# Optimization experiments

Hardware: AMD Instinct MI355X
Metric: run time of the kernel (lower is better)

Reference implementation:

```python
import jax, jax.numpy as jnp
import numpy as np

N_NODES = 50000
N_EDGES = 800000  # includes N_NODES self-loops so every node has in-degree >= 1
D_IN = 64
D_OUT = 64


def setup_inputs() -> dict:
    key = jax.random.key(0)
    k_feat, k_src, k_dst, k_wt, k_wp = jax.random.split(key, 5)
    feat = jax.random.normal(k_feat, (N_NODES, D_IN), dtype=jnp.float32)
    n_rand = N_EDGES - N_NODES
    loops = jnp.arange(N_NODES, dtype=jnp.int64)
    src = jnp.concatenate([loops, jax.random.randint(k_src, (n_rand,), 0, N_NODES, dtype=jnp.int64)])
    dst = jnp.concatenate([loops, jax.random.randint(k_dst, (n_rand,), 0, N_NODES, dtype=jnp.int64)])
    scale = 1.0 / np.sqrt(D_IN)
    W_theta = jax.random.normal(k_wt, (D_IN, D_OUT), dtype=jnp.float32) * scale
    b_theta = jnp.zeros((D_OUT,), dtype=jnp.float32)
    W_phi = jax.random.normal(k_wp, (D_IN, D_OUT), dtype=jnp.float32) * scale
    b_phi = jnp.zeros((D_OUT,), dtype=jnp.float32)
    return {"feat": feat, "src": src, "dst": dst,
            "W_theta": W_theta, "b_theta": b_theta,
            "W_phi": W_phi, "b_phi": b_phi}


def reference(feat, src, dst, W_theta, b_theta, W_phi, b_phi):
    # Per-edge message: theta(x_dst - x_src)  [fn.v_sub_u then Dense theta]
    diff = feat[dst] - feat[src]                       # [E, D_in]
    theta_e = diff @ W_theta + b_theta                 # [E, D_out]
    # Per-destination-node term: phi(x_dst)  [Dense phi]
    phi = feat @ W_phi + b_phi                         # [N, D_out]
    e = theta_e + phi[dst]                             # [E, D_out]  (fn.e_add_v)
    # Scatter-max aggregation by destination node (fn.max)
    out = jax.ops.segment_max(e, dst, num_segments=feat.shape[0])  # [N, D_out]
    return out
```

## Files before the change

### kernel.cpp

```cpp
#include <hip/hip_runtime.h>
#include <hip/hip_bf16.h>

#define N_NODES 50000
#define N_EDGES 800000
#define D 64
#define NB 1563
#define BCAP 1024
#define CHUNK_E 2048
#define NSC 391
#define NSTRIP 3125
#define GEMM_BLKS 196
#define NWAVES 784
#define SPW 4
#define MSTR 65

typedef __attribute__((ext_vector_type(8))) short short8v;
typedef __attribute__((ext_vector_type(4))) float float4v;

__device__ __forceinline__ float b2f(unsigned short h) {
    return __uint_as_float(((unsigned)h) << 16);
}
__device__ __forceinline__ unsigned short f2b(float f) {
    __hip_bfloat16 t = __float2bfloat16(f);
    return *reinterpret_cast<unsigned short*>(&t);
}
__device__ __forceinline__ short f2bs(float f) { return (short)f2b(f); }
__device__ __forceinline__ unsigned f2ord(float f) {
    unsigned u = __float_as_uint(f);
    return (u & 0x80000000u) ? ~u : (u | 0x80000000u);
}
__device__ __forceinline__ float ord2f(unsigned o) {
    return __uint_as_float((o & 0x80000000u) ? (o ^ 0x80000000u) : ~o);
}

__global__ __launch_bounds__(256)
void setup(const void* __restrict__ featv, const void* __restrict__ srcv,
           const void* __restrict__ Wtv, const void* __restrict__ btv,
           const void* __restrict__ Wpv, const void* __restrict__ bpv,
           unsigned* __restrict__ flags, unsigned* __restrict__ c_cur,
           unsigned short* __restrict__ WTfrag, unsigned short* __restrict__ WPfrag,
           float* __restrict__ bias_sum) {
    __shared__ unsigned sf[2];
    const int t = threadIdx.x;
    if (t < 64) {
        const unsigned short* p = (const unsigned short*)featv;
        float x = b2f(p[2 * t]);
        float a = fabsf(x);
        bool insane = !(a <= 64.f) || (x != 0.f && a < 9.3132e-10f);
        unsigned long long m = __ballot(insane);
        if (t == 0) sf[0] = (__popcll(m) >= 8) ? 1u : 0u;
    } else if (t < 128) {
        const int* s32 = (const int*)srcv;
        int v = s32[2 * (t - 64) + 1];
        unsigned long long m = __ballot(v == 0);
        if (t == 64) sf[1] = (__popcll(m) >= 32) ? 1u : 0u;
    }
    __syncthreads();
    const unsigned fp32mode = sf[0];
    if (t < 2) flags[t] = sf[t];
    for (int i = t; i < NB; i += 256) c_cur[i] = 0;
#pragma unroll
    for (int i = 0; i < 16; ++i) {
        int e = i * 256 + t;
        int k = e >> 6, n = e & 63;
        float vt, vp;
        if (fp32mode) {
            vt = ((const float*)Wtv)[e];
            vp = ((const float*)Wpv)[e];
        } else {
            vt = b2f(((const unsigned short*)Wtv)[e]);
            vp = b2f(((const unsigned short*)Wpv)[e]);
        }
        WTfrag[n * 64 + k] = f2b(vt);
        WPfrag[n * 64 + k] = f2b(vp);
    }
    if (t < 64) {
        if (fp32mode)
            bias_sum[t] = ((const float*)btv)[t] + ((const float*)bpv)[t];
        else
            bias_sum[t] = b2f(((const unsigned short*)btv)[t])
                        + b2f(((const unsigned short*)bpv)[t]);
    }
}

__device__ __forceinline__ void loadA_bf16(const short* F, int w, int m, int q,
                                           short8v& A0, short8v& A1) {
    const short* fr = F + (w * 16 + m) * D + q * 8;
    A0 = *(const short8v*)fr;
    A1 = *(const short8v*)(fr + 32);
}
__device__ __forceinline__ void loadA_raw(const float* F, int w, int m, int q,
                                          float4 r[8]) {
    const float* fr = F + (w * 16 + m) * D + q * 8;
    r[0] = *(const float4*)(fr);      r[1] = *(const float4*)(fr + 4);
    r[2] = *(const float4*)(fr + 32); r[3] = *(const float4*)(fr + 36);
}
__device__ __forceinline__ void cvtA(const float4 r[8], short8v& A0, short8v& A1) {
    A0 = (short8v){f2bs(r[0].x), f2bs(r[0].y), f2bs(r[0].z), f2bs(r[0].w),
                   f2bs(r[1].x), f2bs(r[1].y), f2bs(r[1].z), f2bs(r[1].w)};
    A1 = (short8v){f2bs(r[2].x), f2bs(r[2].y), f2bs(r[2].z), f2bs(r[2].w),
                   f2bs(r[3].x), f2bs(r[3].y), f2bs(r[3].z), f2bs(r[3].w)};
}

__global__ __launch_bounds__(256)
void gemm_scatter(const void* __restrict__ featv,
                  const unsigned short* __restrict__ WTfrag,
                  const unsigned short* __restrict__ WPfrag,
                  const float* __restrict__ bias_sum,
                  const void* __restrict__ srcv, const void* __restrict__ dstv,
                  const unsigned* __restrict__ flags,
                  unsigned* __restrict__ c_cur, unsigned* __restrict__ packed,
                  unsigned short* __restrict__ T16, void* __restrict__ outv) {
    const unsigned fp32mode = flags[0];
    if (blockIdx.x < GEMM_BLKS) {
        const int lane = threadIdx.x & 63;
        const int wid  = threadIdx.x >> 6;
        const int wave = blockIdx.x * 4 + wid;
        const int m = lane & 15, q = lane >> 4;

        const short8v* BT = (const short8v*)WTfrag;
        const short8v* BP = (const short8v*)WPfrag;
        short8v Wt0[4], Wt1[4], Wp0[4], Wp1[4];
        float4 bs4[4];
#pragma unroll
        for (int c = 0; c < 4; ++c) {
            const int col = 16 * c + m;
            Wt0[c] = BT[col * 8 + q];
            Wt1[c] = BT[col * 8 + 4 + q];
            Wp0[c] = BP[col * 8 + q];
            Wp1[c] = BP[col * 8 + 4 + q];
            bs4[c] = *(const float4*)(bias_sum + 16 * c + 4 * q);
        }

        float* Cf  = (float*)outv;
        unsigned short* Ch = (unsigned short*)outv;
        const float* Ff = (const float*)featv;
        const short* Fh = (const short*)featv;

        short8v A0, A1;
        float4 raw[8];
        int w = wave;
        if (fp32mode) { loadA_raw(Ff, min(w, NSTRIP - 1), m, q, raw); cvtA(raw, A0, A1); }
        else          loadA_bf16(Fh, min(w, NSTRIP - 1), m, q, A0, A1);

#pragma unroll
        for (int s = 0; s < SPW; ++s) {
            const int wn = wave + (s + 1) * NWAVES;
            if (s + 1 < SPW) {
                if (fp32mode) loadA_raw(Ff, min(wn, NSTRIP - 1), m, q, raw);
                else          loadA_bf16(Fh, min(wn, NSTRIP - 1), m, q, A0, A1);
            }
            if (w < NSTRIP) {
                short8v Acur0, Acur1;
                if (s + 1 < SPW && !fp32mode) {
                    loadA_bf16(Fh, w, m, q, Acur0, Acur1);
                } else {
                    Acur0 = A0; Acur1 = A1;
                }
                const int node = w * 16 + m;
                unsigned short* Trow = T16 + node * D;
#pragma unroll
                for (int c = 0; c < 4; ++c) {
                    float4v accT = (float4v){0.f, 0.f, 0.f, 0.f};
                    float4v accP = (float4v){bs4[c].x, bs4[c].y, bs4[c].z, bs4[c].w};
                    accT = __builtin_amdgcn_mfma_f32_16x16x32_bf16(Wt0[c], Acur0, accT, 0, 0, 0);
                    accT = __builtin_amdgcn_mfma_f32_16x16x32_bf16(Wt1[c], Acur1, accT, 0, 0, 0);
                    accP = __builtin_amdgcn_mfma_f32_16x16x32_bf16(Wp0[c], Acur0, accP, 0, 0, 0);
                    accP = __builtin_amdgcn_mfma_f32_16x16x32_bf16(Wp1[c], Acur1, accP, 0, 0, 0);
                    const int foff = 16 * c + 4 * q;
                    unsigned t0 = (unsigned)f2b(accT[0]) | ((unsigned)f2b(accT[1]) << 16);
                    unsigned t1 = (unsigned)f2b(accT[2]) | ((unsigned)f2b(accT[3]) << 16);
                    *(uint2*)(Trow + foff) = make_uint2(t0, t1);
                    if (fp32mode) {
                        *(float4*)(Cf + node * D + foff) =
                            make_float4(accT[0] + accP[0], accT[1] + accP[1],
                                        accT[2] + accP[2], accT[3] + accP[3]);
                    } else {
                        unsigned c0 = (unsigned)f2b(accT[0] + accP[0])
                                    | ((unsigned)f2b(accT[1] + accP[1]) << 16);
                        unsigned c1 = (unsigned)f2b(accT[2] + accP[2])
                                    | ((unsigned)f2b(accT[3] + accP[3]) << 16);
                        *(uint2*)(Ch + node * D + foff) = make_uint2(c0, c1);
                    }
                }
            }
            w = wn;
            if (fp32mode && s + 1 < SPW) cvtA(raw, A0, A1);
        }
    } else {
        __shared__ unsigned h[NB];
        const int t = threadIdx.x;
        for (int i = t; i < NB; i += 256) h[i] = 0;
        __syncthreads();
        const unsigned idx64 = flags[1];
        const int base = (blockIdx.x - GEMM_BLKS) * CHUNK_E;
        unsigned pk[CHUNK_E / 256];
#pragma unroll
        for (int j = 0; j < CHUNK_E / 256; ++j) {
            int e = base + j * 256 + t;
            unsigned p = 0xFFFFFFFFu;
            if (e < N_EDGES) {
                int s, d;
                if (idx64) {
                    s = (int)((const long long*)srcv)[e];
                    d = (int)((const long long*)dstv)[e];
                } else {
                    s = ((const int*)srcv)[e];
                    d = ((const int*)dstv)[e];
                }
                s = min(max(s, 0), N_NODES - 1);
                d = min(max(d, 0), N_NODES - 1);
                if (s != d) {
                    p = ((unsigned)d << 16) | (unsigned)s;
                    atomicAdd(&h[d >> 5], 1u);
                }
            }
            pk[j] = p;
        }
        __syncthreads();
        for (int i = t; i < NB; i += 256) {
            unsigned c = h[i];
            h[i] = c ? atomicAdd(&c_cur[i], c) : 0u;
        }
        __syncthreads();
#pragma unroll
        for (int j = 0; j < CHUNK_E / 256; ++j) {
            unsigned p = pk[j];
            if (p != 0xFFFFFFFFu) {
                unsigned bkt = p >> 21;
                unsigned pos = atomicAdd(&h[bkt], 1u);
                if (pos < BCAP)
                    packed[bkt * BCAP + pos] = p;
            }
        }
    }
}

__global__ __launch_bounds__(256, 8)
void bucket_min(const unsigned* __restrict__ c_cur, const unsigned* __restrict__ packed,
                const unsigned short* __restrict__ T16, const unsigned* __restrict__ flags,
                void* __restrict__ outv) {
    __shared__ unsigned mn[32 * MSTR];
    const unsigned fp32mode = flags[0];
    const int t = threadIdx.x;
    const int b = blockIdx.x;
    const int node0 = b << 5;
    for (int sl = t; sl < 32 * 16; sl += 256) {
        const int row = sl >> 4;
        const int f4 = (sl & 15) << 2;
        unsigned* mp = &mn[row * MSTR + f4];
        if (node0 + row < N_NODES) {
            uint2 v = *(const uint2*)(T16 + (node0 + row) * D + f4);
            mp[0] = f2ord(b2f((unsigned short)v.x));
            mp[1] = f2ord(b2f((unsigned short)(v.x >> 16)));
            mp[2] = f2ord(b2f((unsigned short)v.y));
            mp[3] = f2ord(b2f((unsigned short)(v.y >> 16)));
        } else {
            mp[0] = mp[1] = mp[2] = mp[3] = 0xFFFFFFFFu;
        }
    }
    __syncthreads();
    const int cnt = min((int)c_cur[b], BCAP);
    const unsigned* pb = packed + b * BCAP;
    const int lane = t & 63, wv = t >> 6;
    const int g = lane >> 3;
    const int fh = (lane & 7) << 3;
    const int fu = (lane & 7) << 3;
    int i = wv * 8 + g;
    for (; i + 32 < cnt; i += 64) {
        unsigned p0 = pb[i], p1 = pb[i + 32];
        uint4 v0 = *(const uint4*)(T16 + (int)(p0 & 0xFFFFu) * D + fh);
        uint4 v1 = *(const uint4*)(T16 + (int)(p1 & 0xFFFFu) * D + fh);
        unsigned* m0p = &mn[(int)((p0 >> 16) & 31u) * MSTR + fu];
        unsigned* m1p = &mn[(int)((p1 >> 16) & 31u) * MSTR + fu];
        atomicMin(m0p + 0, f2ord(b2f((unsigned short)v0.x)));
        atomicMin(m0p + 1, f2ord(b2f((unsigned short)(v0.x >> 16))));
        atomicMin(m0p + 2, f2ord(b2f((unsigned short)v0.y)));
        atomicMin(m0p + 3, f2ord(b2f((unsigned short)(v0.y >> 16))));
        atomicMin(m0p + 4, f2ord(b2f((unsigned short)v0.z)));
        atomicMin(m0p + 5, f2ord(b2f((unsigned short)(v0.z >> 16))));
        atomicMin(m0p + 6, f2ord(b2f((unsigned short)v0.w)));
        atomicMin(m0p + 7, f2ord(b2f((unsigned short)(v0.w >> 16))));
        atomicMin(m1p + 0, f2ord(b2f((unsigned short)v1.x)));
        atomicMin(m1p + 1, f2ord(b2f((unsigned short)(v1.x >> 16))));
        atomicMin(m1p + 2, f2ord(b2f((unsigned short)v1.y)));
        atomicMin(m1p + 3, f2ord(b2f((unsigned short)(v1.y >> 16))));
        atomicMin(m1p + 4, f2ord(b2f((unsigned short)v1.z)));
        atomicMin(m1p + 5, f2ord(b2f((unsigned short)(v1.z >> 16))));
        atomicMin(m1p + 6, f2ord(b2f((unsigned short)v1.w)));
        atomicMin(m1p + 7, f2ord(b2f((unsigned short)(v1.w >> 16))));
    }
    for (; i < cnt; i += 32) {
        unsigned p0 = pb[i];
        uint4 v0 = *(const uint4*)(T16 + (int)(p0 & 0xFFFFu) * D + fh);
        unsigned* m0p = &mn[(int)((p0 >> 16) & 31u) * MSTR + fu];
        atomicMin(m0p + 0, f2ord(b2f((unsigned short)v0.x)));
        atomicMin(m0p + 1, f2ord(b2f((unsigned short)(v0.x >> 16))));
        atomicMin(m0p + 2, f2ord(b2f((unsigned short)v0.y)));
        atomicMin(m0p + 3, f2ord(b2f((unsigned short)(v0.y >> 16))));
        atomicMin(m0p + 4, f2ord(b2f((unsigned short)v0.z)));
        atomicMin(m0p + 5, f2ord(b2f((unsigned short)(v0.z >> 16))));
        atomicMin(m0p + 6, f2ord(b2f((unsigned short)v0.w)));
        atomicMin(m0p + 7, f2ord(b2f((unsigned short)(v0.w >> 16))));
    }
    __syncthreads();
    for (int sl = t; sl < 32 * 16; sl += 256) {
        const int row = sl >> 4;
        const int node = node0 + row;
        if (node >= N_NODES) continue;
        const int f4 = (sl & 15) << 2;
        const unsigned* mp = &mn[row * MSTR + f4];
        float m0 = ord2f(mp[0]), m1 = ord2f(mp[1]);
        float m2 = ord2f(mp[2]), m3 = ord2f(mp[3]);
        if (fp32mode) {
            float4* C = (float4*)((float*)outv + node * D + f4);
            float4 c = *C;
            *C = make_float4(c.x - m0, c.y - m1, c.z - m2, c.w - m3);
        } else {
            unsigned short* C = (unsigned short*)outv + node * D + f4;
            uint2 c = *(uint2*)C;
            unsigned lo = (unsigned)f2b(b2f((unsigned short)c.x) - m0)
                        | ((unsigned)f2b(b2f((unsigned short)(c.x >> 16)) - m1) << 16);
            unsigned hi = (unsigned)f2b(b2f((unsigned short)c.y) - m2)
                        | ((unsigned)f2b(b2f((unsigned short)(c.y >> 16)) - m3) << 16);
            *(uint2*)C = make_uint2(lo, hi);
        }
    }
}

extern "C" void kernel_launch(void* const* d_in, const int* in_sizes, int n_in,
                              void* d_out, int out_size, void* d_ws, size_t ws_size,
                              hipStream_t stream) {
    char* p = (char*)d_ws;
    unsigned*       flags    = (unsigned*)p;
    unsigned*       c_cur    = (unsigned*)(p + 256);
    unsigned*       packed   = (unsigned*)(p + 8448);
    unsigned short* T16      = (unsigned short*)(p + 8448 + 6402048);
    unsigned short* WTfrag   = (unsigned short*)(p + 8448 + 6402048 + 6400000);
    unsigned short* WPfrag   = (unsigned short*)(p + 8448 + 6402048 + 6400000 + 8192);
    float*          bias_sum = (float*)(p + 8448 + 6402048 + 6400000 + 16384);

    setup<<<1, 256, 0, stream>>>(d_in[0], d_in[1], d_in[3], d_in[4], d_in[5], d_in[6],
                                 flags, c_cur, WTfrag, WPfrag, bias_sum);
    gemm_scatter<<<GEMM_BLKS + NSC, 256, 0, stream>>>(d_in[0], WTfrag, WPfrag, bias_sum,
                                                      d_in[1], d_in[2], flags,
                                                      c_cur, packed, T16, d_out);
    bucket_min<<<NB, 256, 0, stream>>>(c_cur, packed, T16, flags, d_out);
}
```

Baseline: 124.2 us.

## Fuse setup, GEMM/scatter and bucket-min into one cooperative persistent kernel

Replaces the three-kernel sequence with a single cooperative kernel using grid.sync between phases: setup of weight fragments and counters, then GEMM plus edge bucketing, then a dynamic work-queue loop over destination buckets computing the max via LDS atomics. The aim is to remove two kernel launch boundaries and the tail effects between them, and to balance the bucket phase with an atomic cursor. It adds grid-wide barrier cost, limits occupancy to a fixed grid of 1024 blocks, and falls back to the old path if the cooperative launch fails.

```diff
diff --git a/kernel.cpp b/kernel.cpp
--- a/kernel.cpp
+++ b/kernel.cpp
@@ -1,18 +1,25 @@
 #include <hip/hip_runtime.h>
 #include <hip/hip_bf16.h>
+#include <hip/hip_cooperative_groups.h>
+
+namespace cg = cooperative_groups;
 
 #define N_NODES 50000
 #define N_EDGES 800000
 #define D 64
 #define NB 1563
 #define BCAP 1024
+#define NSTRIP 3125
+#define MSTR 65
+#define GRID_B 1024
+#define GEMM_B 391
+#define SCAT_B 633
+#define EPB 1264
 #define CHUNK_E 2048
 #define NSC 391
-#define NSTRIP 3125
 #define GEMM_BLKS 196
 #define NWAVES 784
 #define SPW 4
-#define MSTR 65
 
 typedef __attribute__((ext_vector_type(8))) short short8v;
 typedef __attribute__((ext_vector_type(4))) float float4v;
@@ -31,6 +38,284 @@
 }
 __device__ __forceinline__ float ord2f(unsigned o) {
     return __uint_as_float((o & 0x80000000u) ? (o ^ 0x80000000u) : ~o);
+}
+
+__device__ __forceinline__ void loadA_bf16(const short* F, int w, int m, int q,
+                                           short8v& A0, short8v& A1) {
+    const short* fr = F + (w * 16 + m) * D + q * 8;
+    A0 = *(const short8v*)fr;
+    A1 = *(const short8v*)(fr + 32);
+}
+__device__ __forceinline__ void loadA_raw(const float* F, int w, int m, int q,
+                                          float4 r[8]) {
+    const float* fr = F + (w * 16 + m) * D + q * 8;
+    r[0] = *(const float4*)(fr);      r[1] = *(const float4*)(fr + 4);
+    r[2] = *(const float4*)(fr + 32); r[3] = *(const float4*)(fr + 36);
+}
+__device__ __forceinline__ void cvtA(const float4 r[8], short8v& A0, short8v& A1) {
+    A0 = (short8v){f2bs(r[0].x), f2bs(r[0].y), f2bs(r[0].z), f2bs(r[0].w),
+                   f2bs(r[1].x), f2bs(r[1].y), f2bs(r[1].z), f2bs(r[1].w)};
+    A1 = (short8v){f2bs(r[2].x), f2bs(r[2].y), f2bs(r[2].z), f2bs(r[2].w),
+                   f2bs(r[3].x), f2bs(r[3].y), f2bs(r[3].z), f2bs(r[3].w)};
+}
+
+__global__ __launch_bounds__(256, 4)
+void fused(const void* __restrict__ featv, const void* __restrict__ srcv,
+           const void* __restrict__ dstv, const void* __restrict__ Wtv,
+           const void* __restrict__ btv, const void* __restrict__ Wpv,
+           const void* __restrict__ bpv,
+           unsigned* __restrict__ c_cur, unsigned* __restrict__ packed,
+           unsigned short* __restrict__ T16,
+           unsigned short* __restrict__ WTfrag, unsigned short* __restrict__ WPfrag,
+           float* __restrict__ bias_sum, unsigned* __restrict__ cursor,
+           void* __restrict__ outv) {
+    __shared__ unsigned sh[32 * MSTR];
+    __shared__ unsigned sf[4];
+    cg::grid_group grid = cg::this_grid();
+    const int t = threadIdx.x;
+    const int b = blockIdx.x;
+
+    if (t < 64) {
+        const unsigned short* p = (const unsigned short*)featv;
+        float x = b2f(p[2 * t]);
+        float a = fabsf(x);
+        bool insane = !(a <= 64.f) || (x != 0.f && a < 9.3132e-10f);
+        unsigned long long m = __ballot(insane);
+        if (t == 0) sf[0] = (__popcll(m) >= 8) ? 1u : 0u;
+    } else if (t < 128) {
+        const int* s32 = (const int*)srcv;
+        int v = s32[2 * (t - 64) + 1];
+        unsigned long long m = __ballot(v == 0);
+        if (t == 64) sf[1] = (__popcll(m) >= 32) ? 1u : 0u;
+    }
+    __syncthreads();
+    const unsigned fp32mode = sf[0];
+    const unsigned idx64 = sf[1];
+
+    if (b == 0) {
+#pragma unroll
+        for (int i = 0; i < 16; ++i) {
+            int e = i * 256 + t;
+            int k = e >> 6, n = e & 63;
+            float vt, vp;
+            if (fp32mode) {
+                vt = ((const float*)Wtv)[e];
+                vp = ((const float*)Wpv)[e];
+            } else {
+                vt = b2f(((const unsigned short*)Wtv)[e]);
+                vp = b2f(((const unsigned short*)Wpv)[e]);
+            }
+            WTfrag[n * 64 + k] = f2b(vt);
+            WPfrag[n * 64 + k] = f2b(vp);
+        }
+        if (t < 64) {
+            if (fp32mode)
+                bias_sum[t] = ((const float*)btv)[t] + ((const float*)bpv)[t];
+            else
+                bias_sum[t] = b2f(((const unsigned short*)btv)[t])
+                            + b2f(((const unsigned short*)bpv)[t]);
+        }
+    } else if (b <= 7) {
+        int i = (b - 1) * 256 + t;
+        if (i < NB) c_cur[i] = 0;
+    } else if (b == 8 && t == 0) {
+        *cursor = 0;
+    }
+    grid.sync();
+
+    if (b < GEMM_B) {
+        const int lane = t & 63, wid = t >> 6;
+        const int m = lane & 15, q = lane >> 4;
+        const short8v* BT = (const short8v*)WTfrag;
+        const short8v* BP = (const short8v*)WPfrag;
+        short8v Wt0[4], Wt1[4], Wp0[4], Wp1[4];
+        float4 bs4[4];
+#pragma unroll
+        for (int c = 0; c < 4; ++c) {
+            const int col = 16 * c + m;
+            Wt0[c] = BT[col * 8 + q];
+            Wt1[c] = BT[col * 8 + 4 + q];
+            Wp0[c] = BP[col * 8 + q];
+            Wp1[c] = BP[col * 8 + 4 + q];
+            bs4[c] = *(const float4*)(bias_sum + 16 * c + 4 * q);
+        }
+        float* Cf  = (float*)outv;
+        unsigned short* Ch = (unsigned short*)outv;
+#pragma unroll
+        for (int si = 0; si < 2; ++si) {
+            const int w = b * 8 + wid * 2 + si;
+            if (w < NSTRIP) {
+                short8v A0, A1;
+                if (fp32mode) {
+                    float4 raw[8];
+                    loadA_raw((const float*)featv, w, m, q, raw);
+                    cvtA(raw, A0, A1);
+                } else {
+                    loadA_bf16((const short*)featv, w, m, q, A0, A1);
+                }
+                const int node = w * 16 + m;
+                unsigned short* Trow = T16 + node * D;
+#pragma unroll
+                for (int c = 0; c < 4; ++c) {
+                    float4v accT = (float4v){0.f, 0.f, 0.f, 0.f};
+                    float4v accP = (float4v){bs4[c].x, bs4[c].y, bs4[c].z, bs4[c].w};
+                    accT = __builtin_amdgcn_mfma_f32_16x16x32_bf16(Wt0[c], A0, accT, 0, 0, 0);
+                    accT = __builtin_amdgcn_mfma_f32_16x16x32_bf16(Wt1[c], A1, accT, 0, 0, 0);
+                    accP = __builtin_amdgcn_mfma_f32_16x16x32_bf16(Wp0[c], A0, accP, 0, 0, 0);
+                    accP = __builtin_amdgcn_mfma_f32_16x16x32_bf16(Wp1[c], A1, accP, 0, 0, 0);
+                    const int foff = 16 * c + 4 * q;
+                    unsigned t0 = (unsigned)f2b(accT[0]) | ((unsigned)f2b(accT[1]) << 16);
+                    unsigned t1 = (unsigned)f2b(accT[2]) | ((unsigned)f2b(accT[3]) << 16);
+                    *(uint2*)(Trow + foff) = make_uint2(t0, t1);
+                    if (fp32mode) {
+                        *(float4*)(Cf + node * D + foff) =
+                            make_float4(accT[0] + accP[0], accT[1] + accP[1],
+                                        accT[2] + accP[2], accT[3] + accP[3]);
+                    } else {
+                        unsigned c0 = (unsigned)f2b(accT[0] + accP[0])
+                                    | ((unsigned)f2b(accT[1] + accP[1]) << 16);
+                        unsigned c1 = (unsigned)f2b(accT[2] + accP[2])
+                                    | ((unsigned)f2b(accT[3] + accP[3]) << 16);
+                        *(uint2*)(Ch + node * D + foff) = make_uint2(c0, c1);
+                    }
+                }
+            }
+        }
+    } else {
+        const int base = (b - GEMM_B) * EPB;
+        const int eend = min(base + EPB, N_EDGES);
+        for (int i = t; i < NB; i += 256) sh[i] = 0;
+        __syncthreads();
+        unsigned pk[5];
+#pragma unroll
+        for (int j = 0; j < 5; ++j) {
+            int e = base + j * 256 + t;
+            unsigned p = 0xFFFFFFFFu;
+            if (e < eend) {
+                int s, d;
+                if (idx64) {
+                    s = (int)((const long long*)srcv)[e];
+                    d = (int)((const long long*)dstv)[e];
+                } else {
+                    s = ((const int*)srcv)[e];
+                    d = ((const int*)dstv)[e];
+                }
+                s = min(max(s, 0), N_NODES - 1);
+                d = min(max(d, 0), N_NODES - 1);
+                if (s != d) {
+                    p = ((unsigned)d << 16) | (unsigned)s;
+                    atomicAdd(&sh[d >> 5], 1u);
+                }
+            }
+            pk[j] = p;
+        }
+        __syncthreads();
+        for (int i = t; i < NB; i += 256) {
+            unsigned c = sh[i];
+            sh[i] = c ? atomicAdd(&c_cur[i], c) : 0u;
+        }
+        __syncthreads();
+#pragma unroll
+        for (int j = 0; j < 5; ++j) {
+            unsigned p = pk[j];
+            if (p != 0xFFFFFFFFu) {
+                unsigned bkt = p >> 21;
+                unsigned pos = atomicAdd(&sh[bkt], 1u);
+                if (pos < BCAP)
+                    packed[bkt * BCAP + pos] = p;
+            }
+        }
+    }
+    grid.sync();
+
+    const int lane = t & 63, wv = t >> 6;
+    const int g = lane >> 3;
+    const int fh = (lane & 7) << 3;
+    for (;;) {
+        if (t == 0) sf[2] = atomicAdd(cursor, 1u);
+        __syncthreads();
+        const unsigned bb = sf[2];
+        if (bb >= NB) break;
+        const int node0 = (int)bb << 5;
+        for (int sl = t; sl < 32 * 16; sl += 256) {
+            const int row = sl >> 4;
+            const int f4 = (sl & 15) << 2;
+            unsigned* mp = &sh[row * MSTR + f4];
+            if (node0 + row < N_NODES) {
+                uint2 v = *(const uint2*)(T16 + (node0 + row) * D + f4);
+                mp[0] = f2ord(b2f((unsigned short)v.x));
+                mp[1] = f2ord(b2f((unsigned short)(v.x >> 16)));
+                mp[2] = f2ord(b2f((unsigned short)v.y));
+                mp[3] = f2ord(b2f((unsigned short)(v.y >> 16)));
+            } else {
+                mp[0] = mp[1] = mp[2] = mp[3] = 0xFFFFFFFFu;
+            }
+        }
+        __syncthreads();
+        const int cnt = min((int)c_cur[bb], BCAP);
+        const unsigned* pb = packed + bb * BCAP;
+        int i = wv * 8 + g;
+        for (; i + 32 < cnt; i += 64) {
+            unsigned p0 = pb[i], p1 = pb[i + 32];
+            uint4 v0 = *(const uint4*)(T16 + (int)(p0 & 0xFFFFu) * D + fh);
+            uint4 v1 = *(const uint4*)(T16 + (int)(p1 & 0xFFFFu) * D + fh);
+            unsigned* m0p = &sh[(int)((p0 >> 16) & 31u) * MSTR + fh];
+            unsigned* m1p = &sh[(int)((p1 >> 16) & 31u) * MSTR + fh];
+            atomicMin(m0p + 0, f2ord(b2f((unsigned short)v0.x)));
+            atomicMin(m0p + 1, f2ord(b2f((unsigned short)(v0.x >> 16))));
+            atomicMin(m0p + 2, f2ord(b2f((unsigned short)v0.y)));
+            atomicMin(m0p + 3, f2ord(b2f((unsigned short)(v0.y >> 16))));
+            atomicMin(m0p + 4, f2ord(b2f((unsigned short)v0.z)));
+            atomicMin(m0p + 5, f2ord(b2f((unsigned short)(v0.z >> 16))));
+            atomicMin(m0p + 6, f2ord(b2f((unsigned short)v0.w)));
+            atomicMin(m0p + 7, f2ord(b2f((unsigned short)(v0.w >> 16))));
+            atomicMin(m1p + 0, f2ord(b2f((unsigned short)v1.x)));
+            atomicMin(m1p + 1, f2ord(b2f((unsigned short)(v1.x >> 16))));
+            atomicMin(m1p + 2, f2ord(b2f((unsigned short)v1.y)));
+            atomicMin(m1p + 3, f2ord(b2f((unsigned short)(v1.y >> 16))));
+            atomicMin(m1p + 4, f2ord(b2f((unsigned short)v1.z)));
+            atomicMin(m1p + 5, f2ord(b2f((unsigned short)(v1.z >> 16))));
+            atomicMin(m1p + 6, f2ord(b2f((unsigned short)v1.w)));
+            atomicMin(m1p + 7, f2ord(b2f((unsigned short)(v1.w >> 16))));
+        }
+        for (; i < cnt; i += 32) {
+            unsigned p0 = pb[i];
+            uint4 v0 = *(const uint4*)(T16 + (int)(p0 & 0xFFFFu) * D + fh);
+            unsigned* m0p = &sh[(int)((p0 >> 16) & 31u) * MSTR + fh];
+            atomicMin(m0p + 0, f2ord(b2f((unsigned short)v0.x)));
+            atomicMin(m0p + 1, f2ord(b2f((unsigned short)(v0.x >> 16))));
+            atomicMin(m0p + 2, f2ord(b2f((unsigned short)v0.y)));
+            atomicMin(m0p + 3, f2ord(b2f((unsigned short)(v0.y >> 16))));
+            atomicMin(m0p + 4, f2ord(b2f((unsigned short)v0.z)));
+            atomicMin(m0p + 5, f2ord(b2f((unsigned short)(v0.z >> 16))));
+            atomicMin(m0p + 6, f2ord(b2f((unsigned short)v0.w)));
+            atomicMin(m0p + 7, f2ord(b2f((unsigned short)(v0.w >> 16))));
+        }
+        __syncthreads();
+        for (int sl = t; sl < 32 * 16; sl += 256) {
+            const int row = sl >> 4;
+            const int node = node0 + row;
+            if (node >= N_NODES) continue;
+            const int f4 = (sl & 15) << 2;
+            const unsigned* mp = &sh[row * MSTR + f4];
+            float m0 = ord2f(mp[0]), m1 = ord2f(mp[1]);
+            float m2 = ord2f(mp[2]), m3 = ord2f(mp[3]);
+            if (fp32mode) {
+                float4* C = (float4*)((float*)outv + node * D + f4);
+                float4 c = *C;
+                *C = make_float4(c.x - m0, c.y - m1, c.z - m2, c.w - m3);
+            } else {
+                unsigned short* C = (unsigned short*)outv + node * D + f4;
+                uint2 c = *(uint2*)C;
+                unsigned lo = (unsigned)f2b(b2f((unsigned short)c.x) - m0)
+                            | ((unsigned)f2b(b2f((unsigned short)(c.x >> 16)) - m1) << 16);
+                unsigned hi = (unsigned)f2b(b2f((unsigned short)c.y) - m2)
+                            | ((unsigned)f2b(b2f((unsigned short)(c.y >> 16)) - m3) << 16);
+                *(uint2*)C = make_uint2(lo, hi);
+            }
+        }
+        __syncthreads();
+    }
 }
 
 __global__ __launch_bounds__(256)
@@ -83,25 +368,6 @@
     }
 }
 
-__device__ __forceinline__ void loadA_bf16(const short* F, int w, int m, int q,
-                                           short8v& A0, short8v& A1) {
-    const short* fr = F + (w * 16 + m) * D + q * 8;
-    A0 = *(const short8v*)fr;
-    A1 = *(const short8v*)(fr + 32);
-}
-__device__ __forceinline__ void loadA_raw(const float* F, int w, int m, int q,
-                                          float4 r[8]) {
-    const float* fr = F + (w * 16 + m) * D + q * 8;
-    r[0] = *(const float4*)(fr);      r[1] = *(const float4*)(fr + 4);
-    r[2] = *(const float4*)(fr + 32); r[3] = *(const float4*)(fr + 36);
-}
-__device__ __forceinline__ void cvtA(const float4 r[8], short8v& A0, short8v& A1) {
-    A0 = (short8v){f2bs(r[0].x), f2bs(r[0].y), f2bs(r[0].z), f2bs(r[0].w),
-                   f2bs(r[1].x), f2bs(r[1].y), f2bs(r[1].z), f2bs(r[1].w)};
-    A1 = (short8v){f2bs(r[2].x), f2bs(r[2].y), f2bs(r[2].z), f2bs(r[2].w),
-                   f2bs(r[3].x), f2bs(r[3].y), f2bs(r[3].z), f2bs(r[3].w)};
-}
-
 __global__ __launch_bounds__(256)
 void gemm_scatter(const void* __restrict__ featv,
                   const unsigned short* __restrict__ WTfrag,
@@ -117,7 +383,6 @@
         const int wid  = threadIdx.x >> 6;
         const int wave = blockIdx.x * 4 + wid;
         const int m = lane & 15, q = lane >> 4;
-
         const short8v* BT = (const short8v*)WTfrag;
         const short8v* BP = (const short8v*)WPfrag;
         short8v Wt0[4], Wt1[4], Wp0[4], Wp1[4];
@@ -131,18 +396,15 @@
             Wp1[c] = BP[col * 8 + 4 + q];
             bs4[c] = *(const float4*)(bias_sum + 16 * c + 4 * q);
         }
-
         float* Cf  = (float*)outv;
         unsigned short* Ch = (unsigned short*)outv;
         const float* Ff = (const float*)featv;
         const short* Fh = (const short*)featv;
-
         short8v A0, A1;
         float4 raw[8];
         int w = wave;
         if (fp32mode) { loadA_raw(Ff, min(w, NSTRIP - 1), m, q, raw); cvtA(raw, A0, A1); }
         else          loadA_bf16(Fh, min(w, NSTRIP - 1), m, q, A0, A1);
-
 #pragma unroll
         for (int s = 0; s < SPW; ++s) {
             const int wn = wave + (s + 1) * NWAVES;
@@ -265,14 +527,13 @@
     const int lane = t & 63, wv = t >> 6;
     const int g = lane >> 3;
     const int fh = (lane & 7) << 3;
-    const int fu = (lane & 7) << 3;
     int i = wv * 8 + g;
     for (; i + 32 < cnt; i += 64) {
         unsigned p0 = pb[i], p1 = pb[i + 32];
         uint4 v0 = *(const uint4*)(T16 + (int)(p0 & 0xFFFFu) * D + fh);
         uint4 v1 = *(const uint4*)(T16 + (int)(p1 & 0xFFFFu) * D + fh);
-        unsigned* m0p = &mn[(int)((p0 >> 16) & 31u) * MSTR + fu];
-        unsigned* m1p = &mn[(int)((p1 >> 16) & 31u) * MSTR + fu];
+        unsigned* m0p = &mn[(int)((p0 >> 16) & 31u) * MSTR + fh];
+        unsigned* m1p = &mn[(int)((p1 >> 16) & 31u) * MSTR + fh];
         atomicMin(m0p + 0, f2ord(b2f((unsigned short)v0.x)));
         atomicMin(m0p + 1, f2ord(b2f((unsigned short)(v0.x >> 16))));
         atomicMin(m0p + 2, f2ord(b2f((unsigned short)v0.y)));
@@ -293,7 +554,7 @@
     for (; i < cnt; i += 32) {
         unsigned p0 = pb[i];
         uint4 v0 = *(const uint4*)(T16 + (int)(p0 & 0xFFFFu) * D + fh);
-        unsigned* m0p = &mn[(int)((p0 >> 16) & 31u) * MSTR + fu];
+        unsigned* m0p = &mn[(int)((p0 >> 16) & 31u) * MSTR + fh];
         atomicMin(m0p + 0, f2ord(b2f((unsigned short)v0.x)));
         atomicMin(m0p + 1, f2ord(b2f((unsigned short)(v0.x >> 16))));
         atomicMin(m0p + 2, f2ord(b2f((unsigned short)v0.y)));
@@ -339,11 +600,30 @@
     unsigned short* WTfrag   = (unsigned short*)(p + 8448 + 6402048 + 6400000);
     unsigned short* WPfrag   = (unsigned short*)(p + 8448 + 6402048 + 6400000 + 8192);
     float*          bias_sum = (float*)(p + 8448 + 6402048 + 6400000 + 16384);
-
-    setup<<<1, 256, 0, stream>>>(d_in[0], d_in[1], d_in[3], d_in[4], d_in[5], d_in[6],
-                                 flags, c_cur, WTfrag, WPfrag, bias_sum);
-    gemm_scatter<<<GEMM_BLKS + NSC, 256, 0, stream>>>(d_in[0], WTfrag, WPfrag, bias_sum,
-                                                      d_in[1], d_in[2], flags,
-                                                      c_cur, packed, T16, d_out);
-    bucket_min<<<NB, 256, 0, stream>>>(c_cur, packed, T16, flags, d_out);
-}
+    unsigned*       cursor   = (unsigned*)(p + 8448 + 6402048 + 6400000 + 16640);
+
+    const void* featv = d_in[0];
+    const void* srcv  = d_in[1];
+    const void* dstv  = d_in[2];
+    const void* Wtv   = d_in[3];
+    const void* btv   = d_in[4];
+    const void* Wpv   = d_in[5];
+    const void* bpv   = d_in[6];
+    void* outv = d_out;
+
+    void* kargs[] = { (void*)&featv, (void*)&srcv, (void*)&dstv, (void*)&Wtv,
+                      (void*)&btv, (void*)&Wpv, (void*)&bpv,
+                      (void*)&c_cur, (void*)&packed, (void*)&T16,
+                      (void*)&WTfrag, (void*)&WPfrag, (void*)&bias_sum,
+                      (void*)&cursor, (void*)&outv };
+    hipError_t err = hipLaunchCooperativeKernel((const void*)fused, dim3(GRID_B),
+                                                dim3(256), kargs, 0, stream);
+    if (err != hipSuccess) {
+        setup<<<1, 256, 0, stream>>>(featv, srcv, Wtv, btv, Wpv, bpv,
+                                     flags, c_cur, WTfrag, WPfrag, bias_sum);
+        gemm_scatter<<<GEMM_BLKS + NSC, 256, 0, stream>>>(featv, WTfrag, WPfrag, bias_sum,
+                                                          srcv, dstv, flags,
+                                                          c_cur, packed, T16, outv);
+        bucket_min<<<NB, 256, 0, stream>>>(c_cur, packed, T16, flags, outv);
+    }
+}
```

Result: slower. 340.6 us (+174.2%).

## Fold setup kernel into gemm_scatter and halve scatter block count

Applied to the files above, without the earlier changes.

Removes the single-block setup kernel. Each GEMM block now stages the weights and bias into LDS itself, every block recomputes the dtype/index-width flags locally, and c_cur is zeroed with a memset. This cuts one serialized launch and the global round trip through the weight-fragment buffers. It also doubles the edges per scatter block (half as many blocks) and batches the per-bucket atomicAdd reservations into registers. In exchange, every block repeats the flag detection and weight staging, and with fewer scatter blocks each block does longer serial work.

```diff
diff --git a/kernel.cpp b/kernel.cpp
--- a/kernel.cpp
+++ b/kernel.cpp
@@ -6,13 +6,15 @@
 #define D 64
 #define NB 1563
 #define BCAP 1024
-#define CHUNK_E 2048
-#define NSC 391
+#define CHUNK_E 4096
+#define NSC 196
 #define NSTRIP 3125
 #define GEMM_BLKS 196
 #define NWAVES 784
 #define SPW 4
 #define MSTR 65
+#define WLSTR 72
+#define NRES 7
 
 typedef __attribute__((ext_vector_type(8))) short short8v;
 typedef __attribute__((ext_vector_type(4))) float float4v;
@@ -24,7 +26,6 @@
     __hip_bfloat16 t = __float2bfloat16(f);
     return *reinterpret_cast<unsigned short*>(&t);
 }
-__device__ __forceinline__ short f2bs(float f) { return (short)f2b(f); }
 __device__ __forceinline__ unsigned f2ord(float f) {
     unsigned u = __float_as_uint(f);
     return (u & 0x80000000u) ? ~u : (u | 0x80000000u);
@@ -34,102 +35,80 @@
 }
 
 __global__ __launch_bounds__(256)
-void setup(const void* __restrict__ featv, const void* __restrict__ srcv,
-           const void* __restrict__ Wtv, const void* __restrict__ btv,
-           const void* __restrict__ Wpv, const void* __restrict__ bpv,
-           unsigned* __restrict__ flags, unsigned* __restrict__ c_cur,
-           unsigned short* __restrict__ WTfrag, unsigned short* __restrict__ WPfrag,
-           float* __restrict__ bias_sum) {
+void gemm_scatter(const void* __restrict__ featv,
+                  const void* __restrict__ srcv, const void* __restrict__ dstv,
+                  const void* __restrict__ Wtv, const void* __restrict__ btv,
+                  const void* __restrict__ Wpv, const void* __restrict__ bpv,
+                  unsigned* __restrict__ c_cur, unsigned* __restrict__ packed,
+                  unsigned short* __restrict__ T16, void* __restrict__ outv) {
+    __shared__ __align__(16) unsigned short wt_l[64 * WLSTR];
+    __shared__ __align__(16) unsigned short wp_l[64 * WLSTR];
+    __shared__ __align__(16) float bias_l[64];
+    __shared__ unsigned h[NB];
     __shared__ unsigned sf[2];
     const int t = threadIdx.x;
+
     if (t < 64) {
         const unsigned short* p = (const unsigned short*)featv;
         float x = b2f(p[2 * t]);
         float a = fabsf(x);
         bool insane = !(a <= 64.f) || (x != 0.f && a < 9.3132e-10f);
-        unsigned long long m = __ballot(insane);
-        if (t == 0) sf[0] = (__popcll(m) >= 8) ? 1u : 0u;
+        unsigned long long mm = __ballot(insane);
+        if (t == 0) sf[0] = (__popcll(mm) >= 8) ? 1u : 0u;
     } else if (t < 128) {
         const int* s32 = (const int*)srcv;
         int v = s32[2 * (t - 64) + 1];
-        unsigned long long m = __ballot(v == 0);
-        if (t == 64) sf[1] = (__popcll(m) >= 32) ? 1u : 0u;
+        unsigned long long mm = __ballot(v == 0);
+        if (t == 64) sf[1] = (__popcll(mm) >= 32) ? 1u : 0u;
     }
     __syncthreads();
     const unsigned fp32mode = sf[0];
-    if (t < 2) flags[t] = sf[t];
-    for (int i = t; i < NB; i += 256) c_cur[i] = 0;
-#pragma unroll
-    for (int i = 0; i < 16; ++i) {
-        int e = i * 256 + t;
-        int k = e >> 6, n = e & 63;
-        float vt, vp;
+    const unsigned idx64 = sf[1];
+
+    if (blockIdx.x < GEMM_BLKS) {
         if (fp32mode) {
-            vt = ((const float*)Wtv)[e];
-            vp = ((const float*)Wpv)[e];
+#pragma unroll
+            for (int i = 0; i < 16; ++i) {
+                int e = i * 256 + t;
+                int k = e >> 6, n = e & 63;
+                wt_l[n * WLSTR + k] = f2b(((const float*)Wtv)[e]);
+                wp_l[n * WLSTR + k] = f2b(((const float*)Wpv)[e]);
+            }
         } else {
-            vt = b2f(((const unsigned short*)Wtv)[e]);
-            vp = b2f(((const unsigned short*)Wpv)[e]);
-        }
-        WTfrag[n * 64 + k] = f2b(vt);
-        WPfrag[n * 64 + k] = f2b(vp);
-    }
-    if (t < 64) {
-        if (fp32mode)
-            bias_sum[t] = ((const float*)btv)[t] + ((const float*)bpv)[t];
-        else
-            bias_sum[t] = b2f(((const unsigned short*)btv)[t])
-                        + b2f(((const unsigned short*)bpv)[t]);
-    }
-}
-
-__device__ __forceinline__ void loadA_bf16(const short* F, int w, int m, int q,
-                                           short8v& A0, short8v& A1) {
-    const short* fr = F + (w * 16 + m) * D + q * 8;
-    A0 = *(const short8v*)fr;
-    A1 = *(const short8v*)(fr + 32);
-}
-__device__ __forceinline__ void loadA_raw(const float* F, int w, int m, int q,
-                                          float4 r[8]) {
-    const float* fr = F + (w * 16 + m) * D + q * 8;
-    r[0] = *(const float4*)(fr);      r[1] = *(const float4*)(fr + 4);
-    r[2] = *(const float4*)(fr + 32); r[3] = *(const float4*)(fr + 36);
-}
-__device__ __forceinline__ void cvtA(const float4 r[8], short8v& A0, short8v& A1) {
-    A0 = (short8v){f2bs(r[0].x), f2bs(r[0].y), f2bs(r[0].z), f2bs(r[0].w),
-                   f2bs(r[1].x), f2bs(r[1].y), f2bs(r[1].z), f2bs(r[1].w)};
-    A1 = (short8v){f2bs(r[2].x), f2bs(r[2].y), f2bs(r[2].z), f2bs(r[2].w),
-                   f2bs(r[3].x), f2bs(r[3].y), f2bs(r[3].z), f2bs(r[3].w)};
-}
-
-__global__ __launch_bounds__(256)
-void gemm_scatter(const void* __restrict__ featv,
-                  const unsigned short* __restrict__ WTfrag,
-                  const unsigned short* __restrict__ WPfrag,
-                  const float* __restrict__ bias_sum,
-                  const void* __restrict__ srcv, const void* __restrict__ dstv,
-                  const unsigned* __restrict__ flags,
-                  unsigned* __restrict__ c_cur, unsigned* __restrict__ packed,
-                  unsigned short* __restrict__ T16, void* __restrict__ outv) {
-    const unsigned fp32mode = flags[0];
-    if (blockIdx.x < GEMM_BLKS) {
-        const int lane = threadIdx.x & 63;
-        const int wid  = threadIdx.x >> 6;
+#pragma unroll
+            for (int i = 0; i < 16; ++i) {
+                int e = i * 256 + t;
+                int k = e >> 6, n = e & 63;
+                wt_l[n * WLSTR + k] = ((const unsigned short*)Wtv)[e];
+                wp_l[n * WLSTR + k] = ((const unsigned short*)Wpv)[e];
+            }
+        }
+        if (t < 64) {
+            float bt_, bp_;
+            if (fp32mode) {
+                bt_ = ((const float*)btv)[t];
+                bp_ = ((const float*)bpv)[t];
+            } else {
+                bt_ = b2f(((const unsigned short*)btv)[t]);
+                bp_ = b2f(((const unsigned short*)bpv)[t]);
+            }
+            bias_l[t] = bt_ + bp_;
+        }
+        __syncthreads();
+
+        const int lane = t & 63, wid = t >> 6;
         const int wave = blockIdx.x * 4 + wid;
         const int m = lane & 15, q = lane >> 4;
-
-        const short8v* BT = (const short8v*)WTfrag;
-        const short8v* BP = (const short8v*)WPfrag;
         short8v Wt0[4], Wt1[4], Wp0[4], Wp1[4];
         float4 bs4[4];
 #pragma unroll
         for (int c = 0; c < 4; ++c) {
             const int col = 16 * c + m;
-            Wt0[c] = BT[col * 8 + q];
-            Wt1[c] = BT[col * 8 + 4 + q];
-            Wp0[c] = BP[col * 8 + q];
-            Wp1[c] = BP[col * 8 + 4 + q];
-            bs4[c] = *(const float4*)(bias_sum + 16 * c + 4 * q);
+            Wt0[c] = *(const short8v*)&wt_l[col * WLSTR + q * 8];
+            Wt1[c] = *(const short8v*)&wt_l[col * WLSTR + 32 + q * 8];
+            Wp0[c] = *(const short8v*)&wp_l[col * WLSTR + q * 8];
+            Wp1[c] = *(const short8v*)&wp_l[col * WLSTR + 32 + q * 8];
+            bs4[c] = *(const float4*)&bias_l[16 * c + 4 * q];
         }
 
         float* Cf  = (float*)outv;
@@ -140,20 +119,44 @@
         short8v A0, A1;
         float4 raw[8];
         int w = wave;
-        if (fp32mode) { loadA_raw(Ff, min(w, NSTRIP - 1), m, q, raw); cvtA(raw, A0, A1); }
-        else          loadA_bf16(Fh, min(w, NSTRIP - 1), m, q, A0, A1);
+        {
+            int wc = min(w, NSTRIP - 1);
+            const short* fr = Fh + (wc * 16 + m) * D + q * 8;
+            const float* frf = Ff + (wc * 16 + m) * D + q * 8;
+            if (fp32mode) {
+                raw[0] = *(const float4*)(frf);      raw[1] = *(const float4*)(frf + 4);
+                raw[2] = *(const float4*)(frf + 32); raw[3] = *(const float4*)(frf + 36);
+                A0 = (short8v){(short)f2b(raw[0].x), (short)f2b(raw[0].y), (short)f2b(raw[0].z), (short)f2b(raw[0].w),
+                               (short)f2b(raw[1].x), (short)f2b(raw[1].y), (short)f2b(raw[1].z), (short)f2b(raw[1].w)};
+                A1 = (short8v){(short)f2b(raw[2].x), (short)f2b(raw[2].y), (short)f2b(raw[2].z), (short)f2b(raw[2].w),
+                               (short)f2b(raw[3].x), (short)f2b(raw[3].y), (short)f2b(raw[3].z), (short)f2b(raw[3].w)};
+            } else {
+                A0 = *(const short8v*)fr;
+                A1 = *(const short8v*)(fr + 32);
+            }
+        }
 
 #pragma unroll
         for (int s = 0; s < SPW; ++s) {
             const int wn = wave + (s + 1) * NWAVES;
             if (s + 1 < SPW) {
-                if (fp32mode) loadA_raw(Ff, min(wn, NSTRIP - 1), m, q, raw);
-                else          loadA_bf16(Fh, min(wn, NSTRIP - 1), m, q, A0, A1);
+                int wc = min(wn, NSTRIP - 1);
+                if (fp32mode) {
+                    const float* frf = Ff + (wc * 16 + m) * D + q * 8;
+                    raw[0] = *(const float4*)(frf);      raw[1] = *(const float4*)(frf + 4);
+                    raw[2] = *(const float4*)(frf + 32); raw[3] = *(const float4*)(frf + 36);
+                } else {
+                    const short* fr = Fh + (wc * 16 + m) * D + q * 8;
+                    A0 = *(const short8v*)fr;
+                    A1 = *(const short8v*)(fr + 32);
+                }
             }
             if (w < NSTRIP) {
                 short8v Acur0, Acur1;
                 if (s + 1 < SPW && !fp32mode) {
-                    loadA_bf16(Fh, w, m, q, Acur0, Acur1);
+                    const short* fr = Fh + (w * 16 + m) * D + q * 8;
+                    Acur0 = *(const short8v*)fr;
+                    Acur1 = *(const short8v*)(fr + 32);
                 } else {
                     Acur0 = A0; Acur1 = A1;
                 }
@@ -185,14 +188,16 @@
                 }
             }
             w = wn;
-            if (fp32mode && s + 1 < SPW) cvtA(raw, A0, A1);
+            if (fp32mode && s + 1 < SPW) {
+                A0 = (short8v){(short)f2b(raw[0].x), (short)f2b(raw[0].y), (short)f2b(raw[0].z), (short)f2b(raw[0].w),
+                               (short)f2b(raw[1].x), (short)f2b(raw[1].y), (short)f2b(raw[1].z), (short)f2b(raw[1].w)};
+                A1 = (short8v){(short)f2b(raw[2].x), (short)f2b(raw[2].y), (short)f2b(raw[2].z), (short)f2b(raw[2].w),
+                               (short)f2b(raw[3].x), (short)f2b(raw[3].y), (short)f2b(raw[3].z), (short)f2b(raw[3].w)};
+            }
         }
     } else {
-        __shared__ unsigned h[NB];
-        const int t = threadIdx.x;
         for (int i = t; i < NB; i += 256) h[i] = 0;
         __syncthreads();
-        const unsigned idx64 = flags[1];
         const int base = (blockIdx.x - GEMM_BLKS) * CHUNK_E;
         unsigned pk[CHUNK_E / 256];
 #pragma unroll
@@ -218,9 +223,24 @@
             pk[j] = p;
         }
         __syncthreads();
-        for (int i = t; i < NB; i += 256) {
-            unsigned c = h[i];
-            h[i] = c ? atomicAdd(&c_cur[i], c) : 0u;
+        {
+            unsigned cc[NRES], off[NRES];
+#pragma unroll
+            for (int r = 0; r < NRES; ++r) {
+                int i = r * 256 + t;
+                cc[r] = (i < NB) ? h[i] : 0u;
+            }
+#pragma unroll
+            for (int r = 0; r < NRES; ++r) {
+                int i = r * 256 + t;
+                off[r] = (i < NB && cc[r]) ? atomicAdd(&c_cur[i], cc[r]) : 0u;
+            }
+            __syncthreads();
+#pragma unroll
+            for (int r = 0; r < NRES; ++r) {
+                int i = r * 256 + t;
+                if (i < NB) h[i] = off[r];
+            }
         }
         __syncthreads();
 #pragma unroll
@@ -238,13 +258,21 @@
 
 __global__ __launch_bounds__(256, 8)
 void bucket_min(const unsigned* __restrict__ c_cur, const unsigned* __restrict__ packed,
-                const unsigned short* __restrict__ T16, const unsigned* __restrict__ flags,
+                const unsigned short* __restrict__ T16, const void* __restrict__ featv,
                 void* __restrict__ outv) {
     __shared__ unsigned mn[32 * MSTR];
-    const unsigned fp32mode = flags[0];
+    __shared__ unsigned sf0;
     const int t = threadIdx.x;
     const int b = blockIdx.x;
     const int node0 = b << 5;
+    if (t < 64) {
+        const unsigned short* p = (const unsigned short*)featv;
+        float x = b2f(p[2 * t]);
+        float a = fabsf(x);
+        bool insane = !(a <= 64.f) || (x != 0.f && a < 9.3132e-10f);
+        unsigned long long mm = __ballot(insane);
+        if (t == 0) sf0 = (__popcll(mm) >= 8) ? 1u : 0u;
+    }
     for (int sl = t; sl < 32 * 16; sl += 256) {
         const int row = sl >> 4;
         const int f4 = (sl & 15) << 2;
@@ -260,19 +288,19 @@
         }
     }
     __syncthreads();
+    const unsigned fp32mode = sf0;
     const int cnt = min((int)c_cur[b], BCAP);
     const unsigned* pb = packed + b * BCAP;
     const int lane = t & 63, wv = t >> 6;
     const int g = lane >> 3;
     const int fh = (lane & 7) << 3;
-    const int fu = (lane & 7) << 3;
     int i = wv * 8 + g;
     for (; i + 32 < cnt; i += 64) {
         unsigned p0 = pb[i], p1 = pb[i + 32];
         uint4 v0 = *(const uint4*)(T16 + (int)(p0 & 0xFFFFu) * D + fh);
         uint4 v1 = *(const uint4*)(T16 + (int)(p1 & 0xFFFFu) * D + fh);
-        unsigned* m0p = &mn[(int)((p0 >> 16) & 31u) * MSTR + fu];
-        unsigned* m1p = &mn[(int)((p1 >> 16) & 31u) * MSTR + fu];
+        unsigned* m0p = &mn[(int)((p0 >> 16) & 31u) * MSTR + fh];
+        unsigned* m1p = &mn[(int)((p1 >> 16) & 31u) * MSTR + fh];
         atomicMin(m0p + 0, f2ord(b2f((unsigned short)v0.x)));
         atomicMin(m0p + 1, f2ord(b2f((unsigned short)(v0.x >> 16))));
         atomicMin(m0p + 2, f2ord(b2f((unsigned short)v0.y)));
@@ -293,7 +321,7 @@
     for (; i < cnt; i += 32) {
         unsigned p0 = pb[i];
         uint4 v0 = *(const uint4*)(T16 + (int)(p0 & 0xFFFFu) * D + fh);
-        unsigned* m0p = &mn[(int)((p0 >> 16) & 31u) * MSTR + fu];
+        unsigned* m0p = &mn[(int)((p0 >> 16) & 31u) * MSTR + fh];
         atomicMin(m0p + 0, f2ord(b2f((unsigned short)v0.x)));
         atomicMin(m0p + 1, f2ord(b2f((unsigned short)(v0.x >> 16))));
         atomicMin(m0p + 2, f2ord(b2f((unsigned short)v0.y)));
@@ -328,22 +356,26 @@
     }
 }
 
+__global__ __launch_bounds__(256)
+void zero_ccur(unsigned* __restrict__ c_cur) {
+    int i = blockIdx.x * 256 + threadIdx.x;
+    if (i < NB) c_cur[i] = 0;
+}
+
 extern "C" void kernel_launch(void* const* d_in, const int* in_sizes, int n_in,
                               void* d_out, int out_size, void* d_ws, size_t ws_size,
                               hipStream_t stream) {
     char* p = (char*)d_ws;
-    unsigned*       flags    = (unsigned*)p;
-    unsigned*       c_cur    = (unsigned*)(p + 256);
-    unsigned*       packed   = (unsigned*)(p + 8448);
-    unsigned short* T16      = (unsigned short*)(p + 8448 + 6402048);
-    unsigned short* WTfrag   = (unsigned short*)(p + 8448 + 6402048 + 6400000);
-    unsigned short* WPfrag   = (unsigned short*)(p + 8448 + 6402048 + 6400000 + 8192);
-    float*          bias_sum = (float*)(p + 8448 + 6402048 + 6400000 + 16384);
-
-    setup<<<1, 256, 0, stream>>>(d_in[0], d_in[1], d_in[3], d_in[4], d_in[5], d_in[6],
-                                 flags, c_cur, WTfrag, WPfrag, bias_sum);
-    gemm_scatter<<<GEMM_BLKS + NSC, 256, 0, stream>>>(d_in[0], WTfrag, WPfrag, bias_sum,
-                                                      d_in[1], d_in[2], flags,
+    unsigned*       c_cur  = (unsigned*)p;
+    unsigned*       packed = (unsigned*)(p + 8192);
+    unsigned short* T16    = (unsigned short*)(p + 8192 + 6402048);
+
+    hipError_t e = hipMemsetAsync(c_cur, 0, NB * sizeof(unsigned), stream);
+    if (e != hipSuccess)
+        zero_ccur<<<(NB + 255) / 256, 256, 0, stream>>>(c_cur);
+
+    gemm_scatter<<<GEMM_BLKS + NSC, 256, 0, stream>>>(d_in[0], d_in[1], d_in[2],
+                                                      d_in[3], d_in[4], d_in[5], d_in[6],
                                                       c_cur, packed, T16, d_out);
-    bucket_min<<<NB, 256, 0, stream>>>(c_cur, packed, T16, flags, d_out);
-}
+    bucket_min<<<NB, 256, 0, stream>>>(c_cur, packed, T16, d_in[0], d_out);
+}
```

Measured after the change: 113.4 us. 1.1x faster.
